# Kernel tuning notes

Measured on AMD Instinct MI355X. Metric: run time of the kernel, lower is better.

Reference implementation:

```python
import jax, jax.numpy as jnp
import numpy as np

B, S, D, H = 2, 2048, 1024, 16
DK = D // H

def setup_inputs() -> dict:
    key = jax.random.key(0)
    ks = jax.random.split(key, 12)
    s = 0.02
    inp = {
        'query': jax.random.normal(ks[0], (B, S, D), jnp.float32),
        'key':   jax.random.normal(ks[1], (B, S, D), jnp.float32),
        'value': jax.random.normal(ks[2], (B, S, D), jnp.float32),
        'mask':  jnp.broadcast_to(jnp.tril(jnp.ones((S, S), jnp.int32)), (B, S, S)),
        'wq': jax.random.normal(ks[3], (D, D), jnp.float32) * s,
        'bq': jnp.zeros((D,), jnp.float32),
        'wk': jax.random.normal(ks[4], (D, D), jnp.float32) * s,
        'bk': jnp.zeros((D,), jnp.float32),
        'wv': jax.random.normal(ks[5], (D, D), jnp.float32) * s,
        'bv': jnp.zeros((D,), jnp.float32),
        'wo': jax.random.normal(ks[6], (D, D), jnp.float32) * s,
        'bo': jnp.zeros((D,), jnp.float32),
    }
    return inp

def reference(query, key, value, mask, wq, bq, wk, bk, wv, bv, wo, bo):
    # Linear projections (torch Linear: x @ W.T + b); W stored (out,in)
    Q = query @ wq.T + bq   # (B,Sq,D)
    K = key   @ wk.T + bk   # (B,Sk,D)
    V = value @ wv.T + bv   # (B,Sk,D)
    # split heads -> (B,H,S,DK)
    Q = Q.reshape(B, S, H, DK).transpose(0, 2, 1, 3)
    K = K.reshape(B, S, H, DK).transpose(0, 2, 1, 3)
    V = V.reshape(B, S, H, DK).transpose(0, 2, 1, 3)
    scores = jnp.einsum('bhqd,bhkd->bhqk', Q, K) / jnp.sqrt(jnp.float32(DK))
    scores = jnp.where(mask[:, None, :, :] == 0, -jnp.inf, scores)
    attn = jax.nn.softmax(scores, axis=-1)  # dropout is identity in eval/reference
    context = jnp.einsum('bhqk,bhkd->bhqd', attn, V)
    context = context.transpose(0, 2, 1, 3).reshape(B, S, D)
    return context @ wo.T + bo
```

## Files before the change

kernel.cpp:

```cpp
#include <hip/hip_runtime.h>
#include <hip/hip_bf16.h>


#define B_ 2
#define S_ 2048
#define D_ 1024
#define H_ 16
#define DK_ 64
#define SZX (4096 * 1024)
#define SZW (1024 * 1024)

typedef __attribute__((ext_vector_type(8))) short short8;
typedef __attribute__((ext_vector_type(4))) float f32x4;

using bf16 = __hip_bfloat16;

__device__ __forceinline__ short8 load8(const bf16* p) {
    return *reinterpret_cast<const short8*>(p);
}

__device__ __forceinline__ f32x4 mfma16(short8 a, short8 b, f32x4 c) {
    return __builtin_amdgcn_mfma_f32_16x16x32_bf16(a, b, c, 0, 0, 0);
}

__device__ __forceinline__ void async16(const bf16* g, bf16* l) {
    __builtin_amdgcn_global_load_lds(
        (const __attribute__((address_space(1))) void*)g,
        (__attribute__((address_space(3))) void*)l, 16, 0, 0);
}

__device__ __forceinline__ short bf16rne(float f) {
    unsigned u = __float_as_uint(f);
    return (short)((u + 0x7FFFu + ((u >> 16) & 1u)) >> 16);
}

struct CvtArgs {
    const float* src[7];
    bf16* dst[7];
};

__global__ __launch_bounds__(256) void cvt_kernel(CvtArgs a) {
    const long long e = ((long long)blockIdx.x * 256 + threadIdx.x) * 8;
    int t; long long off;
    if (e < 3LL * SZX) { t = (int)(e >> 22); off = e & (SZX - 1); }
    else { const long long e2 = e - 3LL * SZX; t = 3 + (int)(e2 >> 20); off = e2 & (SZW - 1); }
    const float4 f0 = *reinterpret_cast<const float4*>(a.src[t] + off);
    const float4 f1 = *reinterpret_cast<const float4*>(a.src[t] + off + 4);
    short8 o;
    o[0] = bf16rne(f0.x); o[1] = bf16rne(f0.y); o[2] = bf16rne(f0.z); o[3] = bf16rne(f0.w);
    o[4] = bf16rne(f1.x); o[5] = bf16rne(f1.y); o[6] = bf16rne(f1.z); o[7] = bf16rne(f1.w);
    *reinterpret_cast<short8*>((short*)a.dst[t] + off) = o;
}

struct ProjArgs {
    const bf16* X[3]; const bf16* W[3]; const float* bias[3]; void* Y[3]; int mode[3];
};

__global__ __launch_bounds__(256) void proj_kernel(ProjArgs a) {
    const int z = blockIdx.z;
    const bf16* __restrict__ X = a.X[z];
    const bf16* __restrict__ W = a.W[z];
    const float* __restrict__ bias = a.bias[z];
    const int mode = a.mode[z];

    __shared__ __align__(16) bf16 lA[128 * 64];
    __shared__ __align__(16) bf16 lB[128 * 64];

    const int tid  = threadIdx.x;
    const int wv   = tid >> 6;
    const int lane = tid & 63;
    const int quad = lane >> 4;
    const int l16  = lane & 15;
    const int m0   = blockIdx.x * 128;
    const int n0   = blockIdx.y * 128;
    const int wm   = (wv & 1) * 64;
    const int wn   = (wv >> 1) * 64;

    const int srow  = wv * 8 + (lane >> 3);
    const int sunit = (lane & 7) ^ ((lane >> 3) & 7);
    const bf16* gA = X + (size_t)(m0 + srow) * D_ + sunit * 8;
    const bf16* gB = W + (size_t)(n0 + srow) * D_ + sunit * 8;

    f32x4 acc[4][4] = {};

    #pragma unroll 1
    for (int k0 = 0; k0 < D_; k0 += 64) {
        #pragma unroll
        for (int c = 0; c < 4; ++c) {
            async16(gA + (size_t)c * 32 * D_ + k0, &lA[(c * 32 + wv * 8) * 64]);
            async16(gB + (size_t)c * 32 * D_ + k0, &lB[(c * 32 + wv * 8) * 64]);
        }
        __syncthreads();
        #pragma unroll
        for (int kh = 0; kh < 2; ++kh) {
            short8 af[4], bf_[4];
            #pragma unroll
            for (int ms = 0; ms < 4; ++ms)
                af[ms] = load8(&lA[(wm + ms * 16 + l16) * 64 + (((kh * 4 + quad) ^ (l16 & 7)) * 8)]);
            #pragma unroll
            for (int ns = 0; ns < 4; ++ns)
                bf_[ns] = load8(&lB[(wn + ns * 16 + l16) * 64 + (((kh * 4 + quad) ^ (l16 & 7)) * 8)]);
            #pragma unroll
            for (int ms = 0; ms < 4; ++ms)
                #pragma unroll
                for (int ns = 0; ns < 4; ++ns)
                    acc[ms][ns] = mfma16(af[ms], bf_[ns], acc[ms][ns]);
        }
        __syncthreads();
    }

    #pragma unroll
    for (int ns = 0; ns < 4; ++ns) {
        const int col = n0 + wn + ns * 16 + l16;
        const float bv = bias[col];
        const int h = col >> 6, d = col & 63;
        #pragma unroll
        for (int ms = 0; ms < 4; ++ms) {
            const int rbase = m0 + wm + ms * 16 + quad * 4;
            #pragma unroll
            for (int r = 0; r < 4; ++r) {
                const int m = rbase + r;
                const float val = acc[ms][ns][r] + bv;
                if (mode == 3) {
                    ((float*)a.Y[z])[(size_t)m * D_ + col] = val;
                } else {
                    bf16* Y = (bf16*)a.Y[z];
                    const bf16 o = __float2bfloat16(val);
                    const int b  = m >> 11;
                    const int s  = m & (S_ - 1);
                    const int bh = b * H_ + h;
                    if (mode == 2) Y[((size_t)bh * DK_ + d) * S_ + s] = o;
                    else           Y[((size_t)bh * S_ + s) * DK_ + d] = o;
                }
            }
        }
    }
}

__global__ __launch_bounds__(256) void attn_kernel(
    const bf16* __restrict__ Qb, const bf16* __restrict__ Kb,
    const bf16* __restrict__ Vt, bf16* __restrict__ ctx)
{
    __shared__ __align__(16) bf16 Kt[64 * 64];
    __shared__ __align__(16) bf16 Vl[64 * 64];
    __shared__ __align__(16) bf16 lds_p[4][16][72];

    const int tid  = threadIdx.x;
    const int wv   = tid >> 6;
    const int lane = tid & 63;
    const int quad = lane >> 4;
    const int l16  = lane & 15;
    const int bh   = blockIdx.y;

    const bf16* Qh = Qb + (size_t)bh * (S_ * DK_);
    const bf16* Kh = Kb + (size_t)bh * (S_ * DK_);
    const bf16* Vh = Vt + (size_t)bh * (DK_ * S_);
    const int bb = bh >> 4, hh = bh & 15;

    const float c = 0.18033688011112042f;
    const short8 ones = {16256, 16256, 16256, 16256, 16256, 16256, 16256, 16256};

    const int srow  = wv * 8 + (lane >> 3);
    const int sunit = (lane & 7) ^ ((lane >> 3) & 7);

    #pragma unroll 1
    for (int pass = 0; pass < 2; ++pass) {
        const int q0 = (pass == 0 ? (int)blockIdx.x : 31 - (int)blockIdx.x) * 64;
        const int qr = q0 + wv * 16;

        const short8 qa0 = load8(Qh + (qr + l16) * DK_ + quad * 8);
        const short8 qa1 = load8(Qh + (qr + l16) * DK_ + 32 + quad * 8);

        f32x4 cacc[4] = {};
        f32x4 lsum = {};

        const int ntiles = (q0 >> 6) + 1;
        for (int jt = 0; jt < ntiles; ++jt) {
            const int j0 = jt * 64;

            #pragma unroll
            for (int cc = 0; cc < 2; ++cc) {
                const int r = cc * 32 + srow;
                async16(Kh + (size_t)(j0 + r) * DK_ + sunit * 8, &Kt[(cc * 32 + wv * 8) * 64]);
                async16(Vh + (size_t)r * S_ + j0 + sunit * 8,    &Vl[(cc * 32 + wv * 8) * 64]);
            }
            __syncthreads();

            short8 kb[4][2], vb[4][2];
            #pragma unroll
            for (int t = 0; t < 4; ++t)
                #pragma unroll
                for (int kh = 0; kh < 2; ++kh) {
                    const int u = ((kh * 4 + quad) ^ (l16 & 7)) * 8;
                    kb[t][kh] = load8(&Kt[(t * 16 + l16) * 64 + u]);
                    vb[t][kh] = load8(&Vl[(t * 16 + l16) * 64 + u]);
                }

            f32x4 s[4];
            #pragma unroll
            for (int t = 0; t < 4; ++t) {
                f32x4 zz = {};
                zz = mfma16(qa0, kb[t][0], zz);
                s[t] = mfma16(qa1, kb[t][1], zz);
            }

            #pragma unroll
            for (int r = 0; r < 4; ++r) {
                const int row = qr + quad * 4 + r;
                #pragma unroll
                for (int t = 0; t < 4; ++t) {
                    const float p = (j0 + t * 16 + l16 <= row) ? exp2f(c * s[t][r]) : 0.f;
                    lds_p[wv][quad * 4 + r][t * 16 + l16] = __float2bfloat16(p);
                }
            }

            asm volatile("s_waitcnt lgkmcnt(0)" ::: "memory");
            const short8 pa0 = load8(&lds_p[wv][l16][quad * 8]);
            const short8 pa1 = load8(&lds_p[wv][l16][32 + quad * 8]);

            #pragma unroll
            for (int dt = 0; dt < 4; ++dt) {
                cacc[dt] = mfma16(pa0, vb[dt][0], cacc[dt]);
                cacc[dt] = mfma16(pa1, vb[dt][1], cacc[dt]);
            }
            lsum = mfma16(pa0, ones, lsum);
            lsum = mfma16(pa1, ones, lsum);

            __syncthreads();
        }

        #pragma unroll
        for (int r = 0; r < 4; ++r) {
            const float inv = 1.0f / lsum[r];
            const int row = qr + quad * 4 + r;
            bf16* orow = ctx + (size_t)(bb * S_ + row) * D_ + hh * DK_;
            #pragma unroll
            for (int dt = 0; dt < 4; ++dt)
                orow[dt * 16 + l16] = __float2bfloat16(cacc[dt][r] * inv);
        }
    }
}

extern "C" void kernel_launch(void* const* d_in, const int* in_sizes, int n_in,
                              void* d_out, int out_size, void* d_ws, size_t ws_size,
                              hipStream_t stream) {
    (void)in_sizes; (void)n_in; (void)out_size; (void)ws_size;
    const float* q  = (const float*)d_in[0];
    const float* k  = (const float*)d_in[1];
    const float* v  = (const float*)d_in[2];
    const float* wq = (const float*)d_in[4];
    const float* bq = (const float*)d_in[5];
    const float* wk = (const float*)d_in[6];
    const float* bk = (const float*)d_in[7];
    const float* wv = (const float*)d_in[8];
    const float* bv = (const float*)d_in[9];
    const float* wo = (const float*)d_in[10];
    const float* bo = (const float*)d_in[11];

    bf16* base = (bf16*)d_ws;
    bf16* Qb  = base;
    bf16* Kb  = base + 1 * (size_t)SZX;
    bf16* Vt  = base + 2 * (size_t)SZX;
    bf16* ctx = base + 3 * (size_t)SZX;
    bf16* xq  = base + 4 * (size_t)SZX;
    bf16* xk  = base + 5 * (size_t)SZX;
    bf16* xv  = base + 6 * (size_t)SZX;
    bf16* wqb = base + 7 * (size_t)SZX;
    bf16* wkb = wqb + 1 * (size_t)SZW;
    bf16* wvb = wqb + 2 * (size_t)SZW;
    bf16* wob = wqb + 3 * (size_t)SZW;

    CvtArgs ca;
    ca.src[0] = q;  ca.src[1] = k;  ca.src[2] = v;
    ca.src[3] = wq; ca.src[4] = wk; ca.src[5] = wv; ca.src[6] = wo;
    ca.dst[0] = xq;  ca.dst[1] = xk;  ca.dst[2] = xv;
    ca.dst[3] = wqb; ca.dst[4] = wkb; ca.dst[5] = wvb; ca.dst[6] = wob;
    cvt_kernel<<<8192, 256, 0, stream>>>(ca);

    ProjArgs pa;
    pa.X[0] = xq;  pa.X[1] = xk;  pa.X[2] = xv;
    pa.W[0] = wqb; pa.W[1] = wkb; pa.W[2] = wvb;
    pa.bias[0] = bq; pa.bias[1] = bk; pa.bias[2] = bv;
    pa.Y[0] = Qb; pa.Y[1] = Kb; pa.Y[2] = Vt;
    pa.mode[0] = 0; pa.mode[1] = 1; pa.mode[2] = 2;
    proj_kernel<<<dim3(32, 8, 3), 256, 0, stream>>>(pa);

    attn_kernel<<<dim3(16, 32), 256, 0, stream>>>(Qb, Kb, Vt, ctx);

    ProjArgs po;
    po.X[0] = ctx; po.W[0] = wob; po.bias[0] = bo; po.Y[0] = d_out; po.mode[0] = 3;
    po.X[1] = ctx; po.W[1] = wob; po.bias[1] = bo; po.Y[1] = d_out; po.mode[1] = 3;
    po.X[2] = ctx; po.W[2] = wob; po.bias[2] = bo; po.Y[2] = d_out; po.mode[2] = 3;
    proj_kernel<<<dim3(32, 8, 1), 256, 0, stream>>>(po);
}
```

Measured before the change: 268.7 us.

## Flatten attention grid with heavy-first ordering, skip masks off-diagonal, smaller output-proj tiles

The attention kernel now gives one query tile per block on a 1D grid of 1024 blocks instead of two paired tiles per block. Blocks are ordered longest-first and spread across heads, which lets the hardware scheduler balance the causal triangle. The causal mask compare is now applied only on the diagonal tile, so off-diagonal tiles skip the per-element check. The output projection is templated with a 64-row M tile, doubling its block count to fill more CUs on the small final GEMM, at the cost of less B-tile reuse per block.

```diff
diff --git a/kernel.cpp b/kernel.cpp
--- a/kernel.cpp
+++ b/kernel.cpp
@@ -56,6 +56,7 @@
     const bf16* X[3]; const bf16* W[3]; const float* bias[3]; void* Y[3]; int mode[3];
 };
 
+template <int BM>
 __global__ __launch_bounds__(256) void proj_kernel(ProjArgs a) {
     const int z = blockIdx.z;
     const bf16* __restrict__ X = a.X[z];
@@ -63,7 +64,8 @@
     const float* __restrict__ bias = a.bias[z];
     const int mode = a.mode[z];
 
-    __shared__ __align__(16) bf16 lA[128 * 64];
+    constexpr int MSUB = BM / 32;
+    __shared__ __align__(16) bf16 lA[BM * 64];
     __shared__ __align__(16) bf16 lB[128 * 64];
 
     const int tid  = threadIdx.x;
@@ -71,9 +73,9 @@
     const int lane = tid & 63;
     const int quad = lane >> 4;
     const int l16  = lane & 15;
-    const int m0   = blockIdx.x * 128;
+    const int m0   = blockIdx.x * BM;
     const int n0   = blockIdx.y * 128;
-    const int wm   = (wv & 1) * 64;
+    const int wm   = (wv & 1) * (BM / 2);
     const int wn   = (wv >> 1) * 64;
 
     const int srow  = wv * 8 + (lane >> 3);
@@ -81,27 +83,28 @@
     const bf16* gA = X + (size_t)(m0 + srow) * D_ + sunit * 8;
     const bf16* gB = W + (size_t)(n0 + srow) * D_ + sunit * 8;
 
-    f32x4 acc[4][4] = {};
+    f32x4 acc[MSUB][4] = {};
 
     #pragma unroll 1
     for (int k0 = 0; k0 < D_; k0 += 64) {
         #pragma unroll
-        for (int c = 0; c < 4; ++c) {
+        for (int c = 0; c < MSUB; ++c)
             async16(gA + (size_t)c * 32 * D_ + k0, &lA[(c * 32 + wv * 8) * 64]);
+        #pragma unroll
+        for (int c = 0; c < 4; ++c)
             async16(gB + (size_t)c * 32 * D_ + k0, &lB[(c * 32 + wv * 8) * 64]);
-        }
         __syncthreads();
         #pragma unroll
         for (int kh = 0; kh < 2; ++kh) {
-            short8 af[4], bf_[4];
-            #pragma unroll
-            for (int ms = 0; ms < 4; ++ms)
+            short8 af[MSUB], bf_[4];
+            #pragma unroll
+            for (int ms = 0; ms < MSUB; ++ms)
                 af[ms] = load8(&lA[(wm + ms * 16 + l16) * 64 + (((kh * 4 + quad) ^ (l16 & 7)) * 8)]);
             #pragma unroll
             for (int ns = 0; ns < 4; ++ns)
                 bf_[ns] = load8(&lB[(wn + ns * 16 + l16) * 64 + (((kh * 4 + quad) ^ (l16 & 7)) * 8)]);
             #pragma unroll
-            for (int ms = 0; ms < 4; ++ms)
+            for (int ms = 0; ms < MSUB; ++ms)
                 #pragma unroll
                 for (int ns = 0; ns < 4; ++ns)
                     acc[ms][ns] = mfma16(af[ms], bf_[ns], acc[ms][ns]);
@@ -115,7 +118,7 @@
         const float bv = bias[col];
         const int h = col >> 6, d = col & 63;
         #pragma unroll
-        for (int ms = 0; ms < 4; ++ms) {
+        for (int ms = 0; ms < MSUB; ++ms) {
             const int rbase = m0 + wm + ms * 16 + quad * 4;
             #pragma unroll
             for (int r = 0; r < 4; ++r) {
@@ -150,12 +153,16 @@
     const int lane = tid & 63;
     const int quad = lane >> 4;
     const int l16  = lane & 15;
-    const int bh   = blockIdx.y;
+
+    const int bx = blockIdx.x;
+    const int bh = (bx & 7) * 4 + ((bx >> 3) & 3);
+    const int m  = 31 - (bx >> 5);
+    const int q0 = m * 64;
+    const int qr = q0 + wv * 16;
 
     const bf16* Qh = Qb + (size_t)bh * (S_ * DK_);
     const bf16* Kh = Kb + (size_t)bh * (S_ * DK_);
     const bf16* Vh = Vt + (size_t)bh * (DK_ * S_);
-    const int bb = bh >> 4, hh = bh & 15;
 
     const float c = 0.18033688011112042f;
     const short8 ones = {16256, 16256, 16256, 16256, 16256, 16256, 16256, 16256};
@@ -163,47 +170,49 @@
     const int srow  = wv * 8 + (lane >> 3);
     const int sunit = (lane & 7) ^ ((lane >> 3) & 7);
 
-    #pragma unroll 1
-    for (int pass = 0; pass < 2; ++pass) {
-        const int q0 = (pass == 0 ? (int)blockIdx.x : 31 - (int)blockIdx.x) * 64;
-        const int qr = q0 + wv * 16;
-
-        const short8 qa0 = load8(Qh + (qr + l16) * DK_ + quad * 8);
-        const short8 qa1 = load8(Qh + (qr + l16) * DK_ + 32 + quad * 8);
-
-        f32x4 cacc[4] = {};
-        f32x4 lsum = {};
-
-        const int ntiles = (q0 >> 6) + 1;
-        for (int jt = 0; jt < ntiles; ++jt) {
-            const int j0 = jt * 64;
-
-            #pragma unroll
-            for (int cc = 0; cc < 2; ++cc) {
-                const int r = cc * 32 + srow;
-                async16(Kh + (size_t)(j0 + r) * DK_ + sunit * 8, &Kt[(cc * 32 + wv * 8) * 64]);
-                async16(Vh + (size_t)r * S_ + j0 + sunit * 8,    &Vl[(cc * 32 + wv * 8) * 64]);
+    const short8 qa0 = load8(Qh + (qr + l16) * DK_ + quad * 8);
+    const short8 qa1 = load8(Qh + (qr + l16) * DK_ + 32 + quad * 8);
+
+    f32x4 cacc[4] = {};
+    f32x4 lsum = {};
+
+    for (int jt = 0; jt <= m; ++jt) {
+        const int j0 = jt * 64;
+
+        #pragma unroll
+        for (int cc = 0; cc < 2; ++cc) {
+            const int r = cc * 32 + srow;
+            async16(Kh + (size_t)(j0 + r) * DK_ + sunit * 8, &Kt[(cc * 32 + wv * 8) * 64]);
+            async16(Vh + (size_t)r * S_ + j0 + sunit * 8,    &Vl[(cc * 32 + wv * 8) * 64]);
+        }
+        __syncthreads();
+
+        short8 kb[4][2], vb[4][2];
+        #pragma unroll
+        for (int t = 0; t < 4; ++t)
+            #pragma unroll
+            for (int kh = 0; kh < 2; ++kh) {
+                const int u = ((kh * 4 + quad) ^ (l16 & 7)) * 8;
+                kb[t][kh] = load8(&Kt[(t * 16 + l16) * 64 + u]);
+                vb[t][kh] = load8(&Vl[(t * 16 + l16) * 64 + u]);
             }
-            __syncthreads();
-
-            short8 kb[4][2], vb[4][2];
-            #pragma unroll
-            for (int t = 0; t < 4; ++t)
+
+        f32x4 s[4];
+        #pragma unroll
+        for (int t = 0; t < 4; ++t) {
+            f32x4 zz = {};
+            zz = mfma16(qa0, kb[t][0], zz);
+            s[t] = mfma16(qa1, kb[t][1], zz);
+        }
+
+        if (jt < m) {
+            #pragma unroll
+            for (int r = 0; r < 4; ++r)
                 #pragma unroll
-                for (int kh = 0; kh < 2; ++kh) {
-                    const int u = ((kh * 4 + quad) ^ (l16 & 7)) * 8;
-                    kb[t][kh] = load8(&Kt[(t * 16 + l16) * 64 + u]);
-                    vb[t][kh] = load8(&Vl[(t * 16 + l16) * 64 + u]);
-                }
-
-            f32x4 s[4];
-            #pragma unroll
-            for (int t = 0; t < 4; ++t) {
-                f32x4 zz = {};
-                zz = mfma16(qa0, kb[t][0], zz);
-                s[t] = mfma16(qa1, kb[t][1], zz);
-            }
-
+                for (int t = 0; t < 4; ++t)
+                    lds_p[wv][quad * 4 + r][t * 16 + l16] =
+                        __float2bfloat16(exp2f(c * s[t][r]));
+        } else {
             #pragma unroll
             for (int r = 0; r < 4; ++r) {
                 const int row = qr + quad * 4 + r;
@@ -213,31 +222,32 @@
                     lds_p[wv][quad * 4 + r][t * 16 + l16] = __float2bfloat16(p);
                 }
             }
-
-            asm volatile("s_waitcnt lgkmcnt(0)" ::: "memory");
-            const short8 pa0 = load8(&lds_p[wv][l16][quad * 8]);
-            const short8 pa1 = load8(&lds_p[wv][l16][32 + quad * 8]);
-
-            #pragma unroll
-            for (int dt = 0; dt < 4; ++dt) {
-                cacc[dt] = mfma16(pa0, vb[dt][0], cacc[dt]);
-                cacc[dt] = mfma16(pa1, vb[dt][1], cacc[dt]);
-            }
-            lsum = mfma16(pa0, ones, lsum);
-            lsum = mfma16(pa1, ones, lsum);
-
-            __syncthreads();
-        }
-
-        #pragma unroll
-        for (int r = 0; r < 4; ++r) {
-            const float inv = 1.0f / lsum[r];
-            const int row = qr + quad * 4 + r;
-            bf16* orow = ctx + (size_t)(bb * S_ + row) * D_ + hh * DK_;
-            #pragma unroll
-            for (int dt = 0; dt < 4; ++dt)
-                orow[dt * 16 + l16] = __float2bfloat16(cacc[dt][r] * inv);
-        }
+        }
+
+        asm volatile("s_waitcnt lgkmcnt(0)" ::: "memory");
+        const short8 pa0 = load8(&lds_p[wv][l16][quad * 8]);
+        const short8 pa1 = load8(&lds_p[wv][l16][32 + quad * 8]);
+
+        #pragma unroll
+        for (int dt = 0; dt < 4; ++dt) {
+            cacc[dt] = mfma16(pa0, vb[dt][0], cacc[dt]);
+            cacc[dt] = mfma16(pa1, vb[dt][1], cacc[dt]);
+        }
+        lsum = mfma16(pa0, ones, lsum);
+        lsum = mfma16(pa1, ones, lsum);
+
+        __syncthreads();
+    }
+
+    const int bb = bh >> 4, hh = bh & 15;
+    #pragma unroll
+    for (int r = 0; r < 4; ++r) {
+        const float inv = 1.0f / lsum[r];
+        const int row = qr + quad * 4 + r;
+        bf16* orow = ctx + (size_t)(bb * S_ + row) * D_ + hh * DK_;
+        #pragma unroll
+        for (int dt = 0; dt < 4; ++dt)
+            orow[dt * 16 + l16] = __float2bfloat16(cacc[dt][r] * inv);
     }
 }
 
@@ -283,13 +293,13 @@
     pa.bias[0] = bq; pa.bias[1] = bk; pa.bias[2] = bv;
     pa.Y[0] = Qb; pa.Y[1] = Kb; pa.Y[2] = Vt;
     pa.mode[0] = 0; pa.mode[1] = 1; pa.mode[2] = 2;
-    proj_kernel<<<dim3(32, 8, 3), 256, 0, stream>>>(pa);
-
-    attn_kernel<<<dim3(16, 32), 256, 0, stream>>>(Qb, Kb, Vt, ctx);
+    proj_kernel<128><<<dim3(32, 8, 3), 256, 0, stream>>>(pa);
+
+    attn_kernel<<<dim3(1024), 256, 0, stream>>>(Qb, Kb, Vt, ctx);
 
     ProjArgs po;
     po.X[0] = ctx; po.W[0] = wob; po.bias[0] = bo; po.Y[0] = d_out; po.mode[0] = 3;
     po.X[1] = ctx; po.W[1] = wob; po.bias[1] = bo; po.Y[1] = d_out; po.mode[1] = 3;
     po.X[2] = ctx; po.W[2] = wob; po.bias[2] = bo; po.Y[2] = d_out; po.mode[2] = 3;
-    proj_kernel<<<dim3(32, 8, 1), 256, 0, stream>>>(po);
-}
+    proj_kernel<64><<<dim3(64, 8, 1), 256, 0, stream>>>(po);
+}
```

After: 249.8 us. -7.0%, faster.
